# Optimization experiments

Measured on AMD Instinct MI355X. Metric: run time of the kernel, lower is better.

The kernel has to match this reference:

```python
import jax, jax.numpy as jnp
import numpy as np

B, N, C = 8, 1024, 768
H = 12
HD = C // H  # 64


def setup_inputs() -> dict:
    key = jax.random.key(0)
    k1, k2, k3, k4 = jax.random.split(key, 4)
    x = jax.random.normal(k1, (B, N, C), dtype=jnp.float32)
    # nn.Linear(dim, 3*dim, bias=False): weight shape [3C, C]
    w_qkv = jax.random.normal(k2, (3 * C, C), dtype=jnp.float32) * (C ** -0.5)
    # nn.Linear(dim, dim): weight [C, C], bias [C]
    w_proj = jax.random.normal(k3, (C, C), dtype=jnp.float32) * (C ** -0.5)
    b_proj = jax.random.normal(k4, (C,), dtype=jnp.float32) * 0.01
    return {"x": x, "w_qkv": w_qkv, "w_proj": w_proj, "b_proj": b_proj}


def reference(x, w_qkv, w_proj, b_proj):
    scale = HD ** -0.5
    qkv = jnp.einsum("bnc,dc->bnd", x, w_qkv)  # [B,N,3C]
    qkv = qkv.reshape(B, N, 3, H, HD).transpose(2, 0, 3, 1, 4)  # [3,B,H,N,HD]
    q, k, v = qkv[0], qkv[1], qkv[2]
    attn = jnp.einsum("bhqd,bhkd->bhqk", q, k) * scale  # [B,H,N,N]
    attn = jax.nn.softmax(attn, axis=-1)
    out = jnp.einsum("bhqk,bhkd->bhqd", attn, v)  # [B,H,N,HD]
    out = out.transpose(0, 2, 1, 3).reshape(B, N, C)
    return jnp.einsum("bnc,dc->bnd", out, w_proj) + b_proj
```

## Files before the change

### kernel.cpp

```cpp
#include <hip/hip_runtime.h>
#include <hip/hip_bf16.h>


typedef __attribute__((ext_vector_type(8))) short bf16x8;
typedef __attribute__((ext_vector_type(4))) float f32x4;
typedef __attribute__((ext_vector_type(4))) short s16x4;

static constexpr int BB  = 8;
static constexpr int SEQ = 1024;
static constexpr int CH  = 768;
static constexpr int NH  = 12;
static constexpr int HD  = 64;
static constexpr int MT  = BB * SEQ;
static constexpr int C3  = 3 * CH;

__device__ __forceinline__ float bf2f(short s) {
    unsigned u = ((unsigned)(unsigned short)s) << 16;
    return __builtin_bit_cast(float, u);
}
__device__ __forceinline__ short f2bf(float f) {
    unsigned u = __builtin_bit_cast(unsigned, f);
    u += 0x7FFF + ((u >> 16) & 1);
    return (short)(u >> 16);
}
__device__ __forceinline__ unsigned pack_bf2(float lo, float hi) {
    unsigned ul = __builtin_bit_cast(unsigned, lo) + 0x8000u;
    unsigned uh = __builtin_bit_cast(unsigned, hi) + 0x8000u;
    return __builtin_amdgcn_perm(uh, ul, 0x07060302);
}
__device__ __forceinline__ void async16(const short* g, short* l) {
    __builtin_amdgcn_global_load_lds(
        (const __attribute__((address_space(1))) void*)g,
        (__attribute__((address_space(3))) void*)l, 16, 0, 0);
}

__global__ __launch_bounds__(256) void cvt3(
    const float* __restrict__ a, short* __restrict__ da, int na,
    const float* __restrict__ b, short* __restrict__ db, int nb,
    const float* __restrict__ c, short* __restrict__ dc, int nc)
{
    long i = (long)(blockIdx.x * 256 + threadIdx.x) * 8;
    const float* s; short* d; long off;
    if (i < na)                 { s = a; d = da; off = i; }
    else if (i < (long)na + nb) { s = b; d = db; off = i - na; }
    else                        { s = c; d = dc; off = i - na - nb; }
    float4 x0 = *(const float4*)&s[off];
    float4 x1 = *(const float4*)&s[off + 4];
    bf16x8 o;
    o[0] = f2bf(x0.x); o[1] = f2bf(x0.y); o[2] = f2bf(x0.z); o[3] = f2bf(x0.w);
    o[4] = f2bf(x1.x); o[5] = f2bf(x1.y); o[6] = f2bf(x1.z); o[7] = f2bf(x1.w);
    *(bf16x8*)&d[off] = o;
}

template <bool F32OUT>
__global__ __launch_bounds__(256, 4) void gemm_bt(
    const short* __restrict__ A, const short* __restrict__ Bt,
    const float* __restrict__ bias, void* __restrict__ outp,
    int Ndim, int K)
{
    __shared__ __align__(16) short As[128 * 64];
    __shared__ __align__(16) short Bs[128 * 64];
    const int tid  = threadIdx.x;
    const int wave = tid >> 6, lane = tid & 63;
    const int quad = lane >> 4, l16 = lane & 15;
    const int wr = wave >> 1, wc = wave & 1;
    const int id = blockIdx.x;
    const int xcd = id & 7, t = id >> 3;
    const int row0 = (((t & 7) << 3) | xcd) * 128;
    const int col0 = (t >> 3) * 128;

    f32x4 acc[4][4] = {};

    for (int kb = 0; kb < K; kb += 64) {
        #pragma unroll
        for (int p = 0; p < 4; ++p) {
            int g = p * 256 + wave * 64 + lane;
            int r = g >> 3;
            int cb = ((g & 7) ^ (r & 7)) * 8;
            async16(&A[(long)(row0 + r) * K + kb + cb], &As[(p * 256 + wave * 64) * 8]);
            async16(&Bt[(long)(col0 + r) * K + kb + cb], &Bs[(p * 256 + wave * 64) * 8]);
        }
        __syncthreads();

        #pragma unroll
        for (int kh = 0; kh < 2; ++kh) {
            bf16x8 af[4], bfr[4];
            const int cs = ((kh * 4 + quad) ^ (l16 & 7)) * 8;
            #pragma unroll
            for (int mi = 0; mi < 4; ++mi)
                af[mi] = *(const bf16x8*)&As[(wr * 64 + mi * 16 + l16) * 64 + cs];
            #pragma unroll
            for (int ni = 0; ni < 4; ++ni)
                bfr[ni] = *(const bf16x8*)&Bs[(wc * 64 + ni * 16 + l16) * 64 + cs];
            #pragma unroll
            for (int mi = 0; mi < 4; ++mi)
                #pragma unroll
                for (int ni = 0; ni < 4; ++ni)
                    acc[mi][ni] = __builtin_amdgcn_mfma_f32_16x16x32_bf16(
                        af[mi], bfr[ni], acc[mi][ni], 0, 0, 0);
        }
        __syncthreads();
    }

    #pragma unroll
    for (int mi = 0; mi < 4; ++mi) {
        #pragma unroll
        for (int ni = 0; ni < 4; ++ni) {
            int col = col0 + wc * 64 + ni * 16 + l16;
            float bv = bias ? bias[col] : 0.0f;
            #pragma unroll
            for (int r = 0; r < 4; ++r) {
                int row = row0 + wr * 64 + mi * 16 + quad * 4 + r;
                if (F32OUT)
                    ((float*)outp)[(long)row * Ndim + col] = acc[mi][ni][r] + bv;
                else
                    ((short*)outp)[(long)row * Ndim + col] = f2bf(acc[mi][ni][r] + bv);
            }
        }
    }
}

__global__ __launch_bounds__(256, 3) void attn(
    const short* __restrict__ qkv, short* __restrict__ attout)
{
    constexpr int STK = 72, STV = 68;
    __shared__ __align__(16) short Ks [2][64 * STK];
    __shared__ __align__(16) short Vts[2][64 * STV];
    const int tid  = threadIdx.x;
    const int wave = tid >> 6, lane = tid & 63;
    const int quad = lane >> 4, l16 = lane & 15;
    const int hb = blockIdx.x, h = hb % NH, b = hb / NH;
    const int qbase = blockIdx.y * 128;
    const long base = (long)b * SEQ * C3;

    bf16x8 aq[2][2];
    #pragma unroll
    for (int qt = 0; qt < 2; ++qt) {
        const long qp = base + (long)(qbase + qt * 64 + wave * 16 + l16) * C3 + h * HD;
        aq[qt][0] = *(const bf16x8*)&qkv[qp + quad * 8];
        aq[qt][1] = *(const bf16x8*)&qkv[qp + 32 + quad * 8];
        #pragma unroll
        for (int j = 0; j < 8; ++j) {
            aq[qt][0][j] = f2bf(bf2f(aq[qt][0][j]) * 0.125f);
            aq[qt][1][j] = f2bf(bf2f(aq[qt][1][j]) * 0.125f);
        }
    }

    bf16x8 onesv;
    #pragma unroll
    for (int j = 0; j < 8; ++j) onesv[j] = (short)0x3F80;

    f32x4 acc[2][4] = {};
    f32x4 accl[2] = {};

    const int kr = tid >> 3, kc = (tid & 7) * 8;
    const int vr = tid >> 2, vc = (tid & 3) * 16;
    const short* kp0 = qkv + base + (long)kr * C3 + (CH + h * HD) + kc;
    const short* kp1 = kp0 + (long)32 * C3;
    const short* vp  = qkv + base + (long)vr * C3 + (2 * CH + h * HD) + vc;

    bf16x8 k0r, k1r, v0r, v1r;
    k0r = *(const bf16x8*)kp0;
    k1r = *(const bf16x8*)kp1;
    v0r = *(const bf16x8*)vp;
    v1r = *(const bf16x8*)(vp + 8);

    const int nit = SEQ / 64;
    for (int it = 0; it < nit; ++it) {
        const int bufi = it & 1;
        *(bf16x8*)&Ks[bufi][kr * STK + kc]        = k0r;
        *(bf16x8*)&Ks[bufi][(kr + 32) * STK + kc] = k1r;
        #pragma unroll
        for (int j = 0; j < 8; ++j) {
            Vts[bufi][(vc + j) * STV + vr]     = v0r[j];
            Vts[bufi][(vc + 8 + j) * STV + vr] = v1r[j];
        }
        if (it + 1 < nit) {
            kp0 += (long)64 * C3; kp1 += (long)64 * C3; vp += (long)64 * C3;
            k0r = *(const bf16x8*)kp0;
            k1r = *(const bf16x8*)kp1;
            v0r = *(const bf16x8*)vp;
            v1r = *(const bf16x8*)(vp + 8);
        }
        __syncthreads();
        const short* Kb = Ks[bufi];
        const short* Vb = Vts[bufi];

        #pragma unroll
        for (int qt = 0; qt < 2; ++qt) {
            f32x4 St[4];
            #pragma unroll
            for (int t = 0; t < 4; ++t) {
                bf16x8 k0 = *(const bf16x8*)&Kb[(t * 16 + l16) * STK + quad * 8];
                bf16x8 k1 = *(const bf16x8*)&Kb[(t * 16 + l16) * STK + 32 + quad * 8];
                f32x4 s = {};
                s = __builtin_amdgcn_mfma_f32_16x16x32_bf16(k0, aq[qt][0], s, 0, 0, 0);
                s = __builtin_amdgcn_mfma_f32_16x16x32_bf16(k1, aq[qt][1], s, 0, 0, 0);
                St[t] = s;
            }

            float p[4][4];
            #pragma unroll
            for (int t = 0; t < 4; ++t)
                #pragma unroll
                for (int r = 0; r < 4; ++r) p[t][r] = __expf(St[t][r]);

            #pragma unroll
            for (int kt = 0; kt < 2; ++kt) {
                bf16x8 pf;
                unsigned* pw = (unsigned*)&pf;
                pw[0] = pack_bf2(p[2 * kt][0],     p[2 * kt][1]);
                pw[1] = pack_bf2(p[2 * kt][2],     p[2 * kt][3]);
                pw[2] = pack_bf2(p[2 * kt + 1][0], p[2 * kt + 1][1]);
                pw[3] = pack_bf2(p[2 * kt + 1][2], p[2 * kt + 1][3]);
                accl[qt] = __builtin_amdgcn_mfma_f32_16x16x32_bf16(pf, onesv, accl[qt], 0, 0, 0);
                #pragma unroll
                for (int nb = 0; nb < 4; ++nb) {
                    const short* vrow = &Vb[(nb * 16 + l16) * STV + kt * 32 + quad * 4];
                    bf16x8 vf;
                    *(s16x4*)&vf         = *(const s16x4*)vrow;
                    *(((s16x4*)&vf) + 1) = *(const s16x4*)(vrow + 16);
                    acc[qt][nb] = __builtin_amdgcn_mfma_f32_16x16x32_bf16(pf, vf, acc[qt][nb], 0, 0, 0);
                }
            }
        }
    }

    #pragma unroll
    for (int qt = 0; qt < 2; ++qt) {
        #pragma unroll
        for (int r = 0; r < 4; ++r) {
            float linv = 1.0f / accl[qt][r];
            int row = qbase + qt * 64 + wave * 16 + quad * 4 + r;
            #pragma unroll
            for (int nb = 0; nb < 4; ++nb)
                attout[((long)b * SEQ + row) * CH + h * HD + nb * 16 + l16] =
                    f2bf(acc[qt][nb][r] * linv);
        }
    }
}

extern "C" void kernel_launch(void* const* d_in, const int* in_sizes, int n_in,
                              void* d_out, int out_size, void* d_ws, size_t ws_size,
                              hipStream_t stream) {
    const float* x      = (const float*)d_in[0];
    const float* w_qkv  = (const float*)d_in[1];
    const float* w_proj = (const float*)d_in[2];
    const float* b_proj = (const float*)d_in[3];

    const int nx = MT * CH, nq = C3 * CH, np = CH * CH;

    short* xb      = (short*)d_ws;
    short* wqkvb   = xb + nx;
    short* wprojb  = wqkvb + nq;
    short* qkv     = wprojb + np;
    short* attnout = xb;

    cvt3<<<(nx + nq + np) / 2048, 256, 0, stream>>>(
        x, xb, nx, w_qkv, wqkvb, nq, w_proj, wprojb, np);

    gemm_bt<false><<<64 * (C3 / 128), 256, 0, stream>>>(
        xb, wqkvb, nullptr, qkv, C3, CH);
    attn<<<dim3(96, 8), 256, 0, stream>>>(qkv, attnout);
    gemm_bt<true><<<64 * (CH / 128), 256, 0, stream>>>(
        attnout, wprojb, b_proj, (float*)d_out, CH, CH);
}
```

Measured before the change: 177.4 us.

## Split attention query tile across eight waves of 16 rows each

The attention kernel now launches 512 threads per block instead of 256. Each of eight waves owns 16 query rows, where before each of four waves owned two 16-row tiles. The K/V tile load is spread over twice as many threads, so each thread moves one 8-element chunk of K and one of V. The intent is more waves in flight to hide latency and a lower per-thread register footprint. The cost is that each K/V fragment read from LDS now feeds half as much MFMA work per wave. The aggressive launch bound (512, 6) may also force register limits or spills.

```diff
diff --git a/kernel.cpp b/kernel.cpp
--- a/kernel.cpp
+++ b/kernel.cpp
@@ -120,7 +120,7 @@
     }
 }
 
-__global__ __launch_bounds__(256, 3) void attn(
+__global__ __launch_bounds__(512, 6) void attn(
     const short* __restrict__ qkv, short* __restrict__ attout)
 {
     constexpr int STK = 72, STV = 68;
@@ -133,110 +133,89 @@
     const int qbase = blockIdx.y * 128;
     const long base = (long)b * SEQ * C3;
 
-    bf16x8 aq[2][2];
-    #pragma unroll
-    for (int qt = 0; qt < 2; ++qt) {
-        const long qp = base + (long)(qbase + qt * 64 + wave * 16 + l16) * C3 + h * HD;
-        aq[qt][0] = *(const bf16x8*)&qkv[qp + quad * 8];
-        aq[qt][1] = *(const bf16x8*)&qkv[qp + 32 + quad * 8];
-        #pragma unroll
-        for (int j = 0; j < 8; ++j) {
-            aq[qt][0][j] = f2bf(bf2f(aq[qt][0][j]) * 0.125f);
-            aq[qt][1][j] = f2bf(bf2f(aq[qt][1][j]) * 0.125f);
-        }
+    const long qp = base + (long)(qbase + wave * 16 + l16) * C3 + h * HD;
+    bf16x8 aq0 = *(const bf16x8*)&qkv[qp + quad * 8];
+    bf16x8 aq1 = *(const bf16x8*)&qkv[qp + 32 + quad * 8];
+    #pragma unroll
+    for (int j = 0; j < 8; ++j) {
+        aq0[j] = f2bf(bf2f(aq0[j]) * 0.125f);
+        aq1[j] = f2bf(bf2f(aq1[j]) * 0.125f);
     }
 
     bf16x8 onesv;
     #pragma unroll
     for (int j = 0; j < 8; ++j) onesv[j] = (short)0x3F80;
 
-    f32x4 acc[2][4] = {};
-    f32x4 accl[2] = {};
+    f32x4 acc[4] = {};
+    f32x4 accl = {};
 
     const int kr = tid >> 3, kc = (tid & 7) * 8;
-    const int vr = tid >> 2, vc = (tid & 3) * 16;
-    const short* kp0 = qkv + base + (long)kr * C3 + (CH + h * HD) + kc;
-    const short* kp1 = kp0 + (long)32 * C3;
-    const short* vp  = qkv + base + (long)vr * C3 + (2 * CH + h * HD) + vc;
-
-    bf16x8 k0r, k1r, v0r, v1r;
-    k0r = *(const bf16x8*)kp0;
-    k1r = *(const bf16x8*)kp1;
-    v0r = *(const bf16x8*)vp;
-    v1r = *(const bf16x8*)(vp + 8);
+    const short* kp = qkv + base + (long)kr * C3 + (CH + h * HD) + kc;
+    const short* vp = qkv + base + (long)kr * C3 + (2 * CH + h * HD) + kc;
+
+    bf16x8 kreg = *(const bf16x8*)kp;
+    bf16x8 vreg = *(const bf16x8*)vp;
 
     const int nit = SEQ / 64;
     for (int it = 0; it < nit; ++it) {
         const int bufi = it & 1;
-        *(bf16x8*)&Ks[bufi][kr * STK + kc]        = k0r;
-        *(bf16x8*)&Ks[bufi][(kr + 32) * STK + kc] = k1r;
-        #pragma unroll
-        for (int j = 0; j < 8; ++j) {
-            Vts[bufi][(vc + j) * STV + vr]     = v0r[j];
-            Vts[bufi][(vc + 8 + j) * STV + vr] = v1r[j];
-        }
+        *(bf16x8*)&Ks[bufi][kr * STK + kc] = kreg;
+        #pragma unroll
+        for (int j = 0; j < 8; ++j)
+            Vts[bufi][(kc + j) * STV + kr] = vreg[j];
         if (it + 1 < nit) {
-            kp0 += (long)64 * C3; kp1 += (long)64 * C3; vp += (long)64 * C3;
-            k0r = *(const bf16x8*)kp0;
-            k1r = *(const bf16x8*)kp1;
-            v0r = *(const bf16x8*)vp;
-            v1r = *(const bf16x8*)(vp + 8);
+            kp += (long)64 * C3; vp += (long)64 * C3;
+            kreg = *(const bf16x8*)kp;
+            vreg = *(const bf16x8*)vp;
         }
         __syncthreads();
         const short* Kb = Ks[bufi];
         const short* Vb = Vts[bufi];
 
-        #pragma unroll
-        for (int qt = 0; qt < 2; ++qt) {
-            f32x4 St[4];
-            #pragma unroll
-            for (int t = 0; t < 4; ++t) {
-                bf16x8 k0 = *(const bf16x8*)&Kb[(t * 16 + l16) * STK + quad * 8];
-                bf16x8 k1 = *(const bf16x8*)&Kb[(t * 16 + l16) * STK + 32 + quad * 8];
-                f32x4 s = {};
-                s = __builtin_amdgcn_mfma_f32_16x16x32_bf16(k0, aq[qt][0], s, 0, 0, 0);
-                s = __builtin_amdgcn_mfma_f32_16x16x32_bf16(k1, aq[qt][1], s, 0, 0, 0);
-                St[t] = s;
+        f32x4 St[4];
+        #pragma unroll
+        for (int t = 0; t < 4; ++t) {
+            bf16x8 k0 = *(const bf16x8*)&Kb[(t * 16 + l16) * STK + quad * 8];
+            bf16x8 k1 = *(const bf16x8*)&Kb[(t * 16 + l16) * STK + 32 + quad * 8];
+            f32x4 s = {};
+            s = __builtin_amdgcn_mfma_f32_16x16x32_bf16(k0, aq0, s, 0, 0, 0);
+            s = __builtin_amdgcn_mfma_f32_16x16x32_bf16(k1, aq1, s, 0, 0, 0);
+            St[t] = s;
+        }
+
+        #pragma unroll
+        for (int t = 0; t < 4; ++t)
+            #pragma unroll
+            for (int r = 0; r < 4; ++r) St[t][r] = __expf(St[t][r]);
+
+        #pragma unroll
+        for (int kt = 0; kt < 2; ++kt) {
+            bf16x8 pf;
+            unsigned* pw = (unsigned*)&pf;
+            pw[0] = pack_bf2(St[2 * kt][0],     St[2 * kt][1]);
+            pw[1] = pack_bf2(St[2 * kt][2],     St[2 * kt][3]);
+            pw[2] = pack_bf2(St[2 * kt + 1][0], St[2 * kt + 1][1]);
+            pw[3] = pack_bf2(St[2 * kt + 1][2], St[2 * kt + 1][3]);
+            accl = __builtin_amdgcn_mfma_f32_16x16x32_bf16(pf, onesv, accl, 0, 0, 0);
+            #pragma unroll
+            for (int nb = 0; nb < 4; ++nb) {
+                const short* vrow = &Vb[(nb * 16 + l16) * STV + kt * 32 + quad * 4];
+                bf16x8 vf;
+                *(s16x4*)&vf         = *(const s16x4*)vrow;
+                *(((s16x4*)&vf) + 1) = *(const s16x4*)(vrow + 16);
+                acc[nb] = __builtin_amdgcn_mfma_f32_16x16x32_bf16(pf, vf, acc[nb], 0, 0, 0);
             }
-
-            float p[4][4];
-            #pragma unroll
-            for (int t = 0; t < 4; ++t)
-                #pragma unroll
-                for (int r = 0; r < 4; ++r) p[t][r] = __expf(St[t][r]);
-
-            #pragma unroll
-            for (int kt = 0; kt < 2; ++kt) {
-                bf16x8 pf;
-                unsigned* pw = (unsigned*)&pf;
-                pw[0] = pack_bf2(p[2 * kt][0],     p[2 * kt][1]);
-                pw[1] = pack_bf2(p[2 * kt][2],     p[2 * kt][3]);
-                pw[2] = pack_bf2(p[2 * kt + 1][0], p[2 * kt + 1][1]);
-                pw[3] = pack_bf2(p[2 * kt + 1][2], p[2 * kt + 1][3]);
-                accl[qt] = __builtin_amdgcn_mfma_f32_16x16x32_bf16(pf, onesv, accl[qt], 0, 0, 0);
-                #pragma unroll
-                for (int nb = 0; nb < 4; ++nb) {
-                    const short* vrow = &Vb[(nb * 16 + l16) * STV + kt * 32 + quad * 4];
-                    bf16x8 vf;
-                    *(s16x4*)&vf         = *(const s16x4*)vrow;
-                    *(((s16x4*)&vf) + 1) = *(const s16x4*)(vrow + 16);
-                    acc[qt][nb] = __builtin_amdgcn_mfma_f32_16x16x32_bf16(pf, vf, acc[qt][nb], 0, 0, 0);
-                }
-            }
-        }
-    }
-
-    #pragma unroll
-    for (int qt = 0; qt < 2; ++qt) {
-        #pragma unroll
-        for (int r = 0; r < 4; ++r) {
-            float linv = 1.0f / accl[qt][r];
-            int row = qbase + qt * 64 + wave * 16 + quad * 4 + r;
-            #pragma unroll
-            for (int nb = 0; nb < 4; ++nb)
-                attout[((long)b * SEQ + row) * CH + h * HD + nb * 16 + l16] =
-                    f2bf(acc[qt][nb][r] * linv);
-        }
+        }
+    }
+
+    #pragma unroll
+    for (int r = 0; r < 4; ++r) {
+        float linv = 1.0f / accl[r];
+        int row = qbase + wave * 16 + quad * 4 + r;
+        #pragma unroll
+        for (int nb = 0; nb < 4; ++nb)
+            attout[((long)b * SEQ + row) * CH + h * HD + nb * 16 + l16] =
+                f2bf(acc[nb][r] * linv);
     }
 }
 
@@ -261,7 +240,7 @@
 
     gemm_bt<false><<<64 * (C3 / 128), 256, 0, stream>>>(
         xb, wqkvb, nullptr, qkv, C3, CH);
-    attn<<<dim3(96, 8), 256, 0, stream>>>(qkv, attnout);
+    attn<<<dim3(96, 8), 512, 0, stream>>>(qkv, attnout);
     gemm_bt<true><<<64 * (CH / 128), 256, 0, stream>>>(
         attnout, wprojb, b_proj, (float*)d_out, CH, CH);
 }
```

Result: slower. 181.5 us (+2.3%).
